# Optimization experiments

Hardware: AMD Instinct MI355X
Metric: run time of the kernel (lower is better)

Reference implementation:

```python
import jax, jax.numpy as jnp
import numpy as np

# POLLU: 25 reactions, 20 species. Each flux r_i = k_i * C[a_i] * C[b_i],
# where index 20 points at a constant-ones row (unimolecular reactions).
ONES_ROW = 20
IDX_A = np.array([0, 1, 4, 6, 6, 6, 8, 8, 10, 10, 12, 9, 13, 0, 2, 3, 3, 15, 15, 16, 18, 18, 0, 18, 19], dtype=np.int32)
IDX_B = np.array([ONES_ROW, 3, 1, ONES_ROW, ONES_ROW, 5, ONES_ROW, 5, 1, 0, ONES_ROW, 1, ONES_ROW, 5, ONES_ROW, ONES_ROW, ONES_ROW, ONES_ROW, ONES_ROW, 5, ONES_ROW, ONES_ROW, 3, 0, ONES_ROW], dtype=np.int32)

def _stoich():
    # species -> list of (coef, 1-based reaction id), transcribed from dy0..dy19
    ent = {
        0: [(-1,1),(-1,10),(-1,14),(-1,23),(-1,24),(1,2),(1,3),(1,9),(1,11),(1,12),(1,22),(1,25)],
        1: [(-1,2),(-1,3),(-1,9),(-1,12),(1,1),(1,21)],
        2: [(-1,15),(1,1),(1,17),(1,19),(1,22)],
        3: [(-1,2),(-1,16),(-1,17),(-1,23),(1,15)],
        4: [(-1,3),(2,4),(1,6),(1,7),(1,13),(1,20)],
        5: [(-1,6),(-1,8),(-1,14),(-1,20),(1,3),(2,18)],
        6: [(-1,4),(-1,5),(-1,6),(1,13)],
        7: [(1,4),(1,5),(1,6),(1,7)],
        8: [(-1,7),(-1,8)],
        9: [(-1,12),(1,7),(1,9)],
        10: [(-1,9),(-1,10),(1,8),(1,11)],
        11: [(1,9)],
        12: [(-1,11),(1,10)],
        13: [(-1,13),(1,12)],
        14: [(1,14)],
        15: [(-1,18),(-1,19),(1,16)],
        16: [(-1,20)],
        17: [(1,20)],
        18: [(-1,21),(-1,22),(-1,24),(1,23),(1,25)],
        19: [(-1,25),(1,24)],
    }
    S = np.zeros((20, 25), dtype=np.float32)
    for sp, lst in ent.items():
        for c, r in lst:
            S[sp, r - 1] += c
    return S

S = _stoich()  # [20 species, 25 reactions]
B = 2_000_000


def setup_inputs() -> dict:
    key = jax.random.key(0)
    k1, k2 = jax.random.split(key)
    conc_in = jax.random.uniform(k1, (20, B), dtype=jnp.float32)
    k = jax.random.uniform(k2, (25,), dtype=jnp.float32)
    t = jnp.zeros((1,), dtype=jnp.float32)
    return {"t": t, "conc_in": conc_in, "k": k}


def reference(t, conc_in, k):
    # conc_in: [20, B]. Append ones row so every flux is a product of two gathers.
    C = jnp.concatenate([conc_in, jnp.ones((1, conc_in.shape[1]), conc_in.dtype)], axis=0)  # [21, B]
    flux = k[:, None] * C[IDX_A] * C[IDX_B]  # [25, B]
    dy = jnp.einsum('sr,rb->bs', jnp.asarray(S, dtype=conc_in.dtype), flux)  # [B, 20]
    return dy
```

## Files before the change

kernel.cpp:

```cpp
#include <hip/hip_runtime.h>

#define B_TOTAL 2000000
#define PAD 21

__global__ __launch_bounds__(256) void pollu_kernel(
    const float* __restrict__ conc,
    const float* __restrict__ k,
    float* __restrict__ out)
{
    __shared__ float sk[25];
    __shared__ float lds[256 * PAD];

    if (threadIdx.x < 25) sk[threadIdx.x] = k[threadIdx.x];
    __syncthreads();

    const int t = threadIdx.x;
    const int blockStart = blockIdx.x * 256;
    const int b = blockStart + t;
    const int nvalid = min(256, B_TOTAL - blockStart);

    if (b < B_TOTAL) {
        const size_t B = (size_t)B_TOTAL;
        float c[20];
#pragma unroll
        for (int s = 0; s < 20; ++s) c[s] = conc[(size_t)s * B + (size_t)b];

        const float f1  = sk[0]  * c[0];
        const float f2  = sk[1]  * c[1]  * c[3];
        const float f3  = sk[2]  * c[4]  * c[1];
        const float f4  = sk[3]  * c[6];
        const float f5  = sk[4]  * c[6];
        const float f6  = sk[5]  * c[6]  * c[5];
        const float f7  = sk[6]  * c[8];
        const float f8  = sk[7]  * c[8]  * c[5];
        const float f9  = sk[8]  * c[10] * c[1];
        const float f10 = sk[9]  * c[10] * c[0];
        const float f11 = sk[10] * c[12];
        const float f12 = sk[11] * c[9]  * c[1];
        const float f13 = sk[12] * c[13];
        const float f14 = sk[13] * c[0]  * c[5];
        const float f15 = sk[14] * c[2];
        const float f16 = sk[15] * c[3];
        const float f17 = sk[16] * c[3];
        const float f18 = sk[17] * c[15];
        const float f19 = sk[18] * c[15];
        const float f20 = sk[19] * c[16] * c[5];
        const float f21 = sk[20] * c[18];
        const float f22 = sk[21] * c[18];
        const float f23 = sk[22] * c[0]  * c[3];
        const float f24 = sk[23] * c[18] * c[0];
        const float f25 = sk[24] * c[19];

        float dy[20];
        dy[0]  = -f1 - f10 - f14 - f23 - f24 + f2 + f3 + f9 + f11 + f12 + f22 + f25;
        dy[1]  = -f2 - f3 - f9 - f12 + f1 + f21;
        dy[2]  = -f15 + f1 + f17 + f19 + f22;
        dy[3]  = -f2 - f16 - f17 - f23 + f15;
        dy[4]  = -f3 + 2.0f * f4 + f6 + f7 + f13 + f20;
        dy[5]  = -f6 - f8 - f14 - f20 + f3 + 2.0f * f18;
        dy[6]  = -f4 - f5 - f6 + f13;
        dy[7]  =  f4 + f5 + f6 + f7;
        dy[8]  = -f7 - f8;
        dy[9]  = -f12 + f7 + f9;
        dy[10] = -f9 - f10 + f8 + f11;
        dy[11] =  f9;
        dy[12] = -f11 + f10;
        dy[13] = -f13 + f12;
        dy[14] =  f14;
        dy[15] = -f18 - f19 + f16;
        dy[16] = -f20;
        dy[17] =  f20;
        dy[18] = -f21 - f22 - f24 + f23 + f25;
        dy[19] = -f25 + f24;

#pragma unroll
        for (int s = 0; s < 20; ++s) lds[t * PAD + s] = dy[s];
    }
    __syncthreads();

    float4* outv = (float4*)out;
    const int blockBaseF4 = blockIdx.x * 1280;
    const int nF4 = nvalid * 5;
#pragma unroll
    for (int i = 0; i < 5; ++i) {
        const int J = i * 256 + t;
        if (J < nF4) {
            const int q = J / 5;
            const int r = 4 * (J % 5);
            const float* p = &lds[q * PAD + r];
            outv[blockBaseF4 + J] = make_float4(p[0], p[1], p[2], p[3]);
        }
    }
}

extern "C" void kernel_launch(void* const* d_in, const int* in_sizes, int n_in,
                              void* d_out, int out_size, void* d_ws, size_t ws_size,
                              hipStream_t stream) {
    const float* conc = (const float*)d_in[1];
    const float* k    = (const float*)d_in[2];
    float* out        = (float*)d_out;

    const int block = 256;
    const int grid  = (B_TOTAL + block - 1) / block;
    pollu_kernel<<<grid, block, 0, stream>>>(conc, k, out);
}
```

Measured before the change: 272.5 us.

## Process four columns per thread with float4 loads and staged LDS transpose

```diff
diff --git a/kernel.cpp b/kernel.cpp
--- a/kernel.cpp
+++ b/kernel.cpp
@@ -1,94 +1,123 @@
 #include <hip/hip_runtime.h>
 
 #define B_TOTAL 2000000
-#define PAD 21
+#define RS 260
+#define CPB 1024
 
 __global__ __launch_bounds__(256) void pollu_kernel(
     const float* __restrict__ conc,
     const float* __restrict__ k,
     float* __restrict__ out)
 {
-    __shared__ float sk[25];
-    __shared__ float lds[256 * PAD];
-
-    if (threadIdx.x < 25) sk[threadIdx.x] = k[threadIdx.x];
-    __syncthreads();
+    __shared__ __align__(16) float lds[20 * RS];
 
     const int t = threadIdx.x;
-    const int blockStart = blockIdx.x * 256;
-    const int b = blockStart + t;
-    const int nvalid = min(256, B_TOTAL - blockStart);
+    const int base = blockIdx.x * CPB;
+    const int ncols = min(CPB, B_TOTAL - base);
 
-    if (b < B_TOTAL) {
-        const size_t B = (size_t)B_TOTAL;
-        float c[20];
+    const float k0 = k[0],  k1 = k[1],  k2 = k[2],  k3 = k[3],  k4 = k[4];
+    const float k5 = k[5],  k6 = k[6],  k7 = k[7],  k8 = k[8],  k9 = k[9];
+    const float k10 = k[10], k11 = k[11], k12 = k[12], k13 = k[13], k14 = k[14];
+    const float k15 = k[15], k16 = k[16], k17 = k[17], k18 = k[18], k19 = k[19];
+    const float k20 = k[20], k21 = k[21], k22 = k[22], k23 = k[23], k24 = k[24];
+
+#define POLLU_FLUX_DY(C)                                                      \
+        const float f1  = k0  * C(0);                                         \
+        const float f2  = k1  * C(1)  * C(3);                                 \
+        const float f3  = k2  * C(4)  * C(1);                                 \
+        const float f4  = k3  * C(6);                                         \
+        const float f5  = k4  * C(6);                                         \
+        const float f6  = k5  * C(6)  * C(5);                                 \
+        const float f7  = k6  * C(8);                                         \
+        const float f8  = k7  * C(8)  * C(5);                                 \
+        const float f9  = k8  * C(10) * C(1);                                 \
+        const float f10 = k9  * C(10) * C(0);                                 \
+        const float f11 = k10 * C(12);                                        \
+        const float f12 = k11 * C(9)  * C(1);                                 \
+        const float f13 = k12 * C(13);                                        \
+        const float f14 = k13 * C(0)  * C(5);                                 \
+        const float f15 = k14 * C(2);                                         \
+        const float f16 = k15 * C(3);                                         \
+        const float f17 = k16 * C(3);                                         \
+        const float f18 = k17 * C(15);                                        \
+        const float f19 = k18 * C(15);                                        \
+        const float f20 = k19 * C(16) * C(5);                                 \
+        const float f21 = k20 * C(18);                                        \
+        const float f22 = k21 * C(18);                                        \
+        const float f23 = k22 * C(0)  * C(3);                                 \
+        const float f24 = k23 * C(18) * C(0);                                 \
+        const float f25 = k24 * C(19);                                        \
+        C(0)  = -f1 - f10 - f14 - f23 - f24 + f2 + f3 + f9 + f11 + f12 + f22 + f25; \
+        C(1)  = -f2 - f3 - f9 - f12 + f1 + f21;                               \
+        C(2)  = -f15 + f1 + f17 + f19 + f22;                                  \
+        C(3)  = -f2 - f16 - f17 - f23 + f15;                                  \
+        C(4)  = -f3 + 2.0f * f4 + f6 + f7 + f13 + f20;                        \
+        C(5)  = -f6 - f8 - f14 - f20 + f3 + 2.0f * f18;                       \
+        C(6)  = -f4 - f5 - f6 + f13;                                          \
+        C(7)  =  f4 + f5 + f6 + f7;                                           \
+        C(8)  = -f7 - f8;                                                     \
+        C(9)  = -f12 + f7 + f9;                                               \
+        C(10) = -f9 - f10 + f8 + f11;                                         \
+        C(11) =  f9;                                                          \
+        C(12) = -f11 + f10;                                                   \
+        C(13) = -f13 + f12;                                                   \
+        C(14) =  f14;                                                         \
+        C(15) = -f18 - f19 + f16;                                             \
+        C(16) = -f20;                                                         \
+        C(17) =  f20;                                                         \
+        C(18) = -f21 - f22 - f24 + f23 + f25;                                 \
+        C(19) = -f25 + f24;
+
+#define CX(s) c4[s].x
+#define CY(s) c4[s].y
+#define CZ(s) c4[s].z
+#define CW(s) c4[s].w
+#define CA(s) c[s]
+
+    if (ncols == CPB) {
+        float4 c4[20];
+        const size_t off = (size_t)base + (size_t)(4 * t);
 #pragma unroll
-        for (int s = 0; s < 20; ++s) c[s] = conc[(size_t)s * B + (size_t)b];
+        for (int s = 0; s < 20; ++s)
+            c4[s] = *(const float4*)(conc + (size_t)s * B_TOTAL + off);
 
-        const float f1  = sk[0]  * c[0];
-        const float f2  = sk[1]  * c[1]  * c[3];
-        const float f3  = sk[2]  * c[4]  * c[1];
-        const float f4  = sk[3]  * c[6];
-        const float f5  = sk[4]  * c[6];
-        const float f6  = sk[5]  * c[6]  * c[5];
-        const float f7  = sk[6]  * c[8];
-        const float f8  = sk[7]  * c[8]  * c[5];
-        const float f9  = sk[8]  * c[10] * c[1];
-        const float f10 = sk[9]  * c[10] * c[0];
-        const float f11 = sk[10] * c[12];
-        const float f12 = sk[11] * c[9]  * c[1];
-        const float f13 = sk[12] * c[13];
-        const float f14 = sk[13] * c[0]  * c[5];
-        const float f15 = sk[14] * c[2];
-        const float f16 = sk[15] * c[3];
-        const float f17 = sk[16] * c[3];
-        const float f18 = sk[17] * c[15];
-        const float f19 = sk[18] * c[15];
-        const float f20 = sk[19] * c[16] * c[5];
-        const float f21 = sk[20] * c[18];
-        const float f22 = sk[21] * c[18];
-        const float f23 = sk[22] * c[0]  * c[3];
-        const float f24 = sk[23] * c[18] * c[0];
-        const float f25 = sk[24] * c[19];
+        { POLLU_FLUX_DY(CX) }
+        { POLLU_FLUX_DY(CY) }
+        { POLLU_FLUX_DY(CZ) }
+        { POLLU_FLUX_DY(CW) }
 
-        float dy[20];
-        dy[0]  = -f1 - f10 - f14 - f23 - f24 + f2 + f3 + f9 + f11 + f12 + f22 + f25;
-        dy[1]  = -f2 - f3 - f9 - f12 + f1 + f21;
-        dy[2]  = -f15 + f1 + f17 + f19 + f22;
-        dy[3]  = -f2 - f16 - f17 - f23 + f15;
-        dy[4]  = -f3 + 2.0f * f4 + f6 + f7 + f13 + f20;
-        dy[5]  = -f6 - f8 - f14 - f20 + f3 + 2.0f * f18;
-        dy[6]  = -f4 - f5 - f6 + f13;
-        dy[7]  =  f4 + f5 + f6 + f7;
-        dy[8]  = -f7 - f8;
-        dy[9]  = -f12 + f7 + f9;
-        dy[10] = -f9 - f10 + f8 + f11;
-        dy[11] =  f9;
-        dy[12] = -f11 + f10;
-        dy[13] = -f13 + f12;
-        dy[14] =  f14;
-        dy[15] = -f18 - f19 + f16;
-        dy[16] = -f20;
-        dy[17] =  f20;
-        dy[18] = -f21 - f22 - f24 + f23 + f25;
-        dy[19] = -f25 + f24;
-
+        float4* outv = (float4*)out;
+        const int wave = t >> 6;
+        const int lane = t & 63;
 #pragma unroll
-        for (int s = 0; s < 20; ++s) lds[t * PAD + s] = dy[s];
-    }
-    __syncthreads();
-
-    float4* outv = (float4*)out;
-    const int blockBaseF4 = blockIdx.x * 1280;
-    const int nF4 = nvalid * 5;
+        for (int p = 0; p < 4; ++p) {
+            __syncthreads();
+            if (wave == p) {
 #pragma unroll
-    for (int i = 0; i < 5; ++i) {
-        const int J = i * 256 + t;
-        if (J < nF4) {
-            const int q = J / 5;
-            const int r = 4 * (J % 5);
-            const float* p = &lds[q * PAD + r];
-            outv[blockBaseF4 + J] = make_float4(p[0], p[1], p[2], p[3]);
+                for (int s = 0; s < 20; ++s)
+                    *(float4*)&lds[s * RS + 4 * lane] = c4[s];
+            }
+            __syncthreads();
+            const int passBase = blockIdx.x * 5120 + p * 1280;
+#pragma unroll
+            for (int i = 0; i < 5; ++i) {
+                const int J = i * 256 + t;
+                const int q = J / 5;
+                const int r = 4 * (J % 5);
+                outv[passBase + J] = make_float4(lds[(r + 0) * RS + q],
+                                                 lds[(r + 1) * RS + q],
+                                                 lds[(r + 2) * RS + q],
+                                                 lds[(r + 3) * RS + q]);
+            }
+        }
+    } else {
+        for (int col = base + t; col < B_TOTAL; col += 256) {
+            float c[20];
+#pragma unroll
+            for (int s = 0; s < 20; ++s) c[s] = conc[(size_t)s * B_TOTAL + (size_t)col];
+            { POLLU_FLUX_DY(CA) }
+#pragma unroll
+            for (int s = 0; s < 20; ++s) out[(size_t)col * 20 + s] = c[s];
         }
     }
 }
@@ -101,6 +130,6 @@
     float* out        = (float*)d_out;
 
     const int block = 256;
-    const int grid  = (B_TOTAL + block - 1) / block;
+    const int grid  = (B_TOTAL + CPB - 1) / CPB;
     pollu_kernel<<<grid, block, 0, stream>>>(conc, k, out);
 }
```

Result: no change. 277.3 us (+1.8%).
